# Kernel optimization log

Measured on AMD Instinct MI355X. Metric: run time of the kernel, lower is better.

Reference implementation:

```python
import jax, jax.numpy as jnp
import numpy as np

B, L = 8, 2048
AMP, ANG = 48, 16
H = 4
AQK, GQK = 12, 6   # amp/ang qk head dims
AV, GV = 12, 6     # amp/ang v head dims
LOOKBACK = 100


def setup_inputs() -> dict:
    key = jax.random.key(0)
    ks = jax.random.split(key, 16)
    def w(k, i, o):
        # kaiming-uniform-ish scale; stored [in, out] so forward is x @ W
        bound = 1.0 / np.sqrt(i)
        return jax.random.uniform(k, (i, o), jnp.float32, -bound, bound)
    return dict(
        x_ang=jax.random.normal(ks[0], (B, L, 2 * ANG), jnp.float32),
        x_amp=jax.random.normal(ks[1], (B, L, AMP), jnp.float32),
        Wq_amp=w(ks[2], AMP, H * AQK),
        Wk_amp=w(ks[3], AMP, H * AQK),
        Wv_amp=w(ks[4], AMP, H * AV),
        Wq_ang_r=w(ks[5], ANG, H * GQK),
        Wq_ang_i=w(ks[6], ANG, H * GQK),
        Wk_ang_r=w(ks[7], ANG, H * GQK),
        Wk_ang_i=w(ks[8], ANG, H * GQK),
        Wv_ang_r=w(ks[9], ANG, H * GV),
        Wv_ang_i=w(ks[10], ANG, H * GV),
        Wout_amp=w(ks[11], H * AV, AMP),
        bout_amp=jax.random.uniform(ks[12], (AMP,), jnp.float32, -0.1, 0.1),
        Wout_ang_r=w(ks[13], H * GV, ANG),
        Wout_ang_i=w(ks[14], H * GV, ANG),
    )


def _clin(xr, xi, Wr, Wi):
    # complex linear: (xr + i xi) @ (Wr + i Wi)
    return xr @ Wr - xi @ Wi, xr @ Wi + xi @ Wr


def reference(x_ang, x_amp, Wq_amp, Wk_amp, Wv_amp,
              Wq_ang_r, Wq_ang_i, Wk_ang_r, Wk_ang_i,
              Wv_ang_r, Wv_ang_i, Wout_amp, bout_amp,
              Wout_ang_r, Wout_ang_i):
    Bb, Ll, CA = x_ang.shape
    ang_r, ang_i = jnp.split(x_ang, 2, axis=-1)

    def heads(x, hd):  # [B,L,H*hd] -> [B,H,L,hd]
        return x.reshape(Bb, Ll, H, hd).transpose(0, 2, 1, 3)

    q_amp = heads(x_amp @ Wq_amp, AQK)
    k_amp = heads(x_amp @ Wk_amp, AQK)
    qar, qai = _clin(ang_r, ang_i, Wq_ang_r, Wq_ang_i)
    kar, kai = _clin(ang_r, ang_i, Wk_ang_r, Wk_ang_i)
    q = jnp.concatenate([heads(qar, GQK), heads(qai, GQK), q_amp], axis=-1)  # [B,H,L,24]
    k = jnp.concatenate([heads(kar, GQK), heads(kai, GQK), k_amp], axis=-1)

    v_amp = heads(x_amp @ Wv_amp, AV)
    var, vai = _clin(ang_r, ang_i, Wv_ang_r, Wv_ang_i)
    v = jnp.concatenate([heads(var, GV), heads(vai, GV), v_amp], axis=-1)  # [B,H,L,24]

    scale = 1.0 / jnp.sqrt(jnp.asarray(q.shape[-1], q.dtype))
    scores = jnp.einsum('bhqd,bhkd->bhqk', q, k) * scale
    idx = jnp.arange(Ll)
    valid = (idx[None, :] <= idx[:, None]) & (idx[None, :] >= idx[:, None] - (LOOKBACK - 1))
    mask = jnp.where(valid, jnp.asarray(0.0, scores.dtype), jnp.finfo(scores.dtype).min)
    attn = jax.nn.softmax(scores + mask, axis=-1)
    out = jnp.einsum('bhqk,bhkd->bhqd', attn, v)  # [B,H,L,24]

    o_ang_r, o_ang_i, o_amp = jnp.split(out, [GV, 2 * GV], axis=-1)

    def merge(x):  # [B,H,L,hd] -> [B,L,H*hd]
        return x.transpose(0, 2, 1, 3).reshape(Bb, Ll, -1)

    out_amp = merge(o_amp) @ Wout_amp + bout_amp
    out_ang_r, out_ang_i = _clin(merge(o_ang_r), merge(o_ang_i), Wout_ang_r, Wout_ang_i)
    return (out_ang_r, out_ang_i, out_amp)
```

## Files before the change

### kernel.cpp

```cpp
#include <hip/hip_runtime.h>
#include <hip/hip_bf16.h>

constexpr int B = 8;
constexpr int L = 2048;
constexpr int ANG = 16;
constexpr int AMP = 48;
constexpr int H = 4;
constexpr int AQK = 12, GQK = 6;
constexpr int AV = 12, GV = 6;
constexpr int HD = 2 * GQK + AQK;
constexpr int LOOKBACK = 100;
constexpr int NTOK = B * L;

constexpr int TQ     = 64;
constexpr int GROUPS = 4;
constexpr int CHUNK  = 25;
constexpr int MAXK   = TQ + LOOKBACK - 1;
constexpr int NT     = L / TQ;

struct StageT {
    float xam[MAXK][49];
    float xan[MAXK][33];
};
struct TileT {
    float4 Ks[MAXK][8];
    float4 Vs[MAXK][8];
    float4 Qs[TQ][7];
};
union SharedU { StageT stage; TileT t; };

__global__ __launch_bounds__(256, 3) void fused_qkv_attn3_kernel(
    const float* __restrict__ x_ang, const float* __restrict__ x_amp,
    const float* __restrict__ Wq_amp, const float* __restrict__ Wk_amp,
    const float* __restrict__ Wv_amp,
    const float* __restrict__ Wq_ang_r, const float* __restrict__ Wq_ang_i,
    const float* __restrict__ Wk_ang_r, const float* __restrict__ Wk_ang_i,
    const float* __restrict__ Wv_ang_r, const float* __restrict__ Wv_ang_i,
    float* __restrict__ att)
{
    __shared__ SharedU u;

    const int tid = threadIdx.x;
    const int bh  = blockIdx.x / NT;
    const int qt  = blockIdx.x % NT;
    const int b   = bh / H, h = bh % H;
    const int q0  = qt * TQ;
    int kmin = q0 - (LOOKBACK - 1); if (kmin < 0) kmin = 0;
    const int nrows = q0 + TQ - kmin;
    const int qoff  = q0 - kmin;

    {
        const float4* xm4 = (const float4*)(x_amp + ((size_t)b * L + kmin) * AMP);
        const float4* xg4 = (const float4*)(x_ang + ((size_t)b * L + kmin) * (2 * ANG));
        int namp = nrows * 12;
        int ntot = namp + nrows * 8;
        for (int c = tid; c < ntot; c += 256) {
            if (c < namp) {
                int r = c / 12, i = c % 12;
                float4 t = xm4[c];
                float* p = &u.stage.xam[r][4 * i];
                p[0] = t.x; p[1] = t.y; p[2] = t.z; p[3] = t.w;
            } else {
                int c2 = c - namp;
                int r = c2 / 8, i = c2 % 8;
                float4 t = xg4[c2];
                float* p = &u.stage.xan[r][4 * i];
                p[0] = t.x; p[1] = t.y; p[2] = t.z; p[3] = t.w;
            }
        }
    }
    __syncthreads();

    float4 kpack[6], vpack[6], qpack[6];
    const bool kvact = (tid < nrows);
    const bool qact  = (tid >= 192);
    const int  qrow  = tid - 192;

    #pragma unroll
    for (int s = 0; s < 6; ++s) {
        if (kvact) {
            int r = tid;
            if (s >= 3) {
                int col4 = h * AQK + (s - 3) * 4;
                const float* Wk = Wk_amp + col4;
                const float* Wv = Wv_amp + col4;
                float4 ka = {0,0,0,0}, va = {0,0,0,0};
                #pragma unroll
                for (int i = 0; i < AMP; ++i) {
                    float x = u.stage.xam[r][i];
                    float4 wk = *(const float4*)(Wk + i * 48);
                    float4 wv = *(const float4*)(Wv + i * 48);
                    ka.x += x * wk.x; ka.y += x * wk.y; ka.z += x * wk.z; ka.w += x * wk.w;
                    va.x += x * wv.x; va.y += x * wv.y; va.z += x * wv.z; va.w += x * wv.w;
                }
                kpack[s] = ka; vpack[s] = va;
            } else {
                float kk[4], vv[4];
                #pragma unroll
                for (int c = 0; c < 4; ++c) {
                    int d = 4 * s + c;
                    bool re = (d < GQK);
                    int dd = re ? d : d - GQK;
                    int col = h * GQK + dd;
                    const float* WkA = re ? Wk_ang_r : Wk_ang_i;
                    const float* WkB = re ? Wk_ang_i : Wk_ang_r;
                    const float* WvA = re ? Wv_ang_r : Wv_ang_i;
                    const float* WvB = re ? Wv_ang_i : Wv_ang_r;
                    float sgn = re ? -1.f : 1.f;
                    float ak = 0, bk = 0, aw = 0, bw = 0;
                    #pragma unroll
                    for (int i = 0; i < ANG; ++i) {
                        float xr = u.stage.xan[r][i];
                        float xi = u.stage.xan[r][16 + i];
                        ak += xr * WkA[i * 24 + col];  bk += xi * WkB[i * 24 + col];
                        aw += xr * WvA[i * 24 + col];  bw += xi * WvB[i * 24 + col];
                    }
                    kk[c] = ak + sgn * bk;  vv[c] = aw + sgn * bw;
                }
                kpack[s] = make_float4(kk[0], kk[1], kk[2], kk[3]);
                vpack[s] = make_float4(vv[0], vv[1], vv[2], vv[3]);
            }
        }
        if (qact) {
            int r = qoff + qrow;
            if (s >= 3) {
                int col4 = h * AQK + (s - 3) * 4;
                const float* Wq = Wq_amp + col4;
                float4 qa = {0,0,0,0};
                #pragma unroll
                for (int i = 0; i < AMP; ++i) {
                    float x = u.stage.xam[r][i];
                    float4 wq = *(const float4*)(Wq + i * 48);
                    qa.x += x * wq.x; qa.y += x * wq.y; qa.z += x * wq.z; qa.w += x * wq.w;
                }
                qpack[s] = qa;
            } else {
                float qq[4];
                #pragma unroll
                for (int c = 0; c < 4; ++c) {
                    int d = 4 * s + c;
                    bool re = (d < GQK);
                    int dd = re ? d : d - GQK;
                    int col = h * GQK + dd;
                    const float* WA = re ? Wq_ang_r : Wq_ang_i;
                    const float* WB = re ? Wq_ang_i : Wq_ang_r;
                    float sgn = re ? -1.f : 1.f;
                    float aa = 0, bb = 0;
                    #pragma unroll
                    for (int i = 0; i < ANG; ++i) {
                        float xr = u.stage.xan[r][i];
                        float xi = u.stage.xan[r][16 + i];
                        aa += xr * WA[i * 24 + col];  bb += xi * WB[i * 24 + col];
                    }
                    qq[c] = aa + sgn * bb;
                }
                qpack[s] = make_float4(qq[0], qq[1], qq[2], qq[3]);
            }
        }
    }
    __syncthreads();

    if (kvact) {
        int r = tid, rx = r & 7;
        #pragma unroll
        for (int s = 0; s < 6; ++s) {
            u.t.Ks[r][s ^ rx] = kpack[s];
            u.t.Vs[r][s ^ rx] = vpack[s];
        }
    } else if (tid < MAXK) {
        float4 z = make_float4(0.f,0.f,0.f,0.f);
        #pragma unroll
        for (int s = 0; s < 6; ++s) { u.t.Ks[tid][s] = z; u.t.Vs[tid][s] = z; }
    }
    if (qact) {
        #pragma unroll
        for (int s = 0; s < 6; ++s) u.t.Qs[qrow][s] = qpack[s];
    }
    __syncthreads();

    const int lane = tid & 63;
    const int w    = tid >> 6;
    const int q16  = lane & 15;
    const int g    = lane >> 4;
    const int ql   = w * 16 + q16;
    const int qi   = q0 + ql;

    float4 q4[6];
    #pragma unroll
    for (int s = 0; s < 6; ++s) q4[s] = u.t.Qs[ql][s];

    const float scale = 0.2041241452319315f;
    int j0 = qi - (LOOKBACK - 1); if (j0 < 0) j0 = 0;
    const int jstart = j0 + g;

    float sc[CHUNK];
    #pragma unroll
    for (int t = 0; t < CHUNK; ++t) {
        int j  = jstart + t * GROUPS;
        int r  = j - kmin;
        int rx = r & 7;
        float d = 0.f;
        #pragma unroll
        for (int s = 0; s < 6; ++s) {
            float4 kk = u.t.Ks[r][s ^ rx];
            d += q4[s].x*kk.x + q4[s].y*kk.y + q4[s].z*kk.z + q4[s].w*kk.w;
        }
        sc[t] = (j <= qi) ? d * scale : -3.0e38f;
    }
    float m = sc[0];
    #pragma unroll
    for (int t = 1; t < CHUNK; ++t) m = fmaxf(m, sc[t]);
    float ssum = 0.f;
    #pragma unroll
    for (int t = 0; t < CHUNK; ++t) {
        float p = __expf(sc[t] - m);
        p = (sc[t] > -1.0e37f) ? p : 0.f;
        sc[t] = p;
        ssum += p;
    }
    float4 o[6];
    #pragma unroll
    for (int s = 0; s < 6; ++s) o[s] = make_float4(0.f,0.f,0.f,0.f);
    #pragma unroll
    for (int t = 0; t < CHUNK; ++t) {
        float p  = sc[t];
        int j    = jstart + t * GROUPS;
        int r    = j - kmin;
        int rx   = r & 7;
        #pragma unroll
        for (int s = 0; s < 6; ++s) {
            float4 vv = u.t.Vs[r][s ^ rx];
            o[s].x += p * vv.x; o[s].y += p * vv.y;
            o[s].z += p * vv.z; o[s].w += p * vv.w;
        }
    }

    #pragma unroll
    for (int d = 16; d <= 32; d <<= 1) {
        float m2 = __shfl_xor(m, d);
        float s2 = __shfl_xor(ssum, d);
        float mm = fmaxf(m, m2);
        float c1 = __expf(m - mm);
        float c2 = __expf(m2 - mm);
        ssum = ssum * c1 + s2 * c2;
        #pragma unroll
        for (int s = 0; s < 6; ++s) {
            o[s].x = o[s].x * c1 + __shfl_xor(o[s].x, d) * c2;
            o[s].y = o[s].y * c1 + __shfl_xor(o[s].y, d) * c2;
            o[s].z = o[s].z * c1 + __shfl_xor(o[s].z, d) * c2;
            o[s].w = o[s].w * c1 + __shfl_xor(o[s].w, d) * c2;
        }
        m = mm;
    }
    float inv = 1.f / ssum;

    {
        float4* dst = (float4*)att + (size_t)(b * L + qi) * 24 + h * 6;
        if (g == 0) {
            dst[0] = make_float4(o[0].x*inv, o[0].y*inv, o[0].z*inv, o[0].w*inv);
            dst[4] = make_float4(o[4].x*inv, o[4].y*inv, o[4].z*inv, o[4].w*inv);
        } else if (g == 1) {
            dst[1] = make_float4(o[1].x*inv, o[1].y*inv, o[1].z*inv, o[1].w*inv);
            dst[5] = make_float4(o[5].x*inv, o[5].y*inv, o[5].z*inv, o[5].w*inv);
        } else if (g == 2) {
            dst[2] = make_float4(o[2].x*inv, o[2].y*inv, o[2].z*inv, o[2].w*inv);
        } else {
            dst[3] = make_float4(o[3].x*inv, o[3].y*inv, o[3].z*inv, o[3].w*inv);
        }
    }
}

constexpr int PJ_AMP_BLOCKS = (NTOK * 12) / 256;
constexpr int PJ_ANG_BLOCKS = (NTOK * 4) / 256;

__global__ __launch_bounds__(256) void proj4_kernel(
    const float* __restrict__ att,
    const float* __restrict__ Wout_amp, const float* __restrict__ bout_amp,
    const float* __restrict__ Wout_ang_r, const float* __restrict__ Wout_ang_i,
    float* __restrict__ out)
{
    constexpr size_t ANG_OUT = (size_t)NTOK * ANG;
    int bid = blockIdx.x;

    if (bid < PJ_AMP_BLOCKS) {
        int gidx = bid * 256 + threadIdx.x;
        int c4   = (gidx % 12) * 4;
        int tok  = gidx / 12;
        const float4* at4 = (const float4*)att + (size_t)tok * 24;

        float a[48];
        #pragma unroll
        for (int h = 0; h < H; ++h) {
            #pragma unroll
            for (int i = 0; i < 3; ++i) {
                float4 t = at4[h * 6 + 3 + i];
                a[h*12 + 4*i+0]=t.x; a[h*12 + 4*i+1]=t.y;
                a[h*12 + 4*i+2]=t.z; a[h*12 + 4*i+3]=t.w;
            }
        }
        float4 acc = *(const float4*)(bout_amp + c4);
        #pragma unroll
        for (int i = 0; i < 48; ++i) {
            float4 w = *(const float4*)(Wout_amp + i * 48 + c4);
            acc.x += a[i]*w.x; acc.y += a[i]*w.y; acc.z += a[i]*w.z; acc.w += a[i]*w.w;
        }
        *(float4*)(out + 2*ANG_OUT + (size_t)tok * 48 + c4) = acc;
    } else {
        int gidx = (bid - PJ_AMP_BLOCKS) * 256 + threadIdx.x;
        int c4   = (gidx % 4) * 4;
        int tok  = gidx / 4;
        const float4* at4 = (const float4*)att + (size_t)tok * 24;

        float ar[24], ai[24];
        #pragma unroll
        for (int h = 0; h < H; ++h) {
            float4 t0 = at4[h*6+0], t1 = at4[h*6+1], t2 = at4[h*6+2];
            ar[h*6+0]=t0.x; ar[h*6+1]=t0.y; ar[h*6+2]=t0.z; ar[h*6+3]=t0.w;
            ar[h*6+4]=t1.x; ar[h*6+5]=t1.y;
            ai[h*6+0]=t1.z; ai[h*6+1]=t1.w;
            ai[h*6+2]=t2.x; ai[h*6+3]=t2.y; ai[h*6+4]=t2.z; ai[h*6+5]=t2.w;
        }
        float4 accr = make_float4(0.f,0.f,0.f,0.f);
        float4 acci = make_float4(0.f,0.f,0.f,0.f);
        #pragma unroll
        for (int i = 0; i < 24; ++i) {
            float4 wr = *(const float4*)(Wout_ang_r + i * 16 + c4);
            float4 wi = *(const float4*)(Wout_ang_i + i * 16 + c4);
            float r = ar[i], im = ai[i];
            accr.x += r*wr.x - im*wi.x;  accr.y += r*wr.y - im*wi.y;
            accr.z += r*wr.z - im*wi.z;  accr.w += r*wr.w - im*wi.w;
            acci.x += r*wi.x + im*wr.x;  acci.y += r*wi.y + im*wr.y;
            acci.z += r*wi.z + im*wr.z;  acci.w += r*wi.w + im*wr.w;
        }
        *(float4*)(out + (size_t)tok * 16 + c4)           = accr;
        *(float4*)(out + ANG_OUT + (size_t)tok * 16 + c4) = acci;
    }
}

extern "C" void kernel_launch(void* const* d_in, const int* in_sizes, int n_in,
                              void* d_out, int out_size, void* d_ws, size_t ws_size,
                              hipStream_t stream)
{
    const float* x_ang      = (const float*)d_in[0];
    const float* x_amp      = (const float*)d_in[1];
    const float* Wq_amp     = (const float*)d_in[2];
    const float* Wk_amp     = (const float*)d_in[3];
    const float* Wv_amp     = (const float*)d_in[4];
    const float* Wq_ang_r   = (const float*)d_in[5];
    const float* Wq_ang_i   = (const float*)d_in[6];
    const float* Wk_ang_r   = (const float*)d_in[7];
    const float* Wk_ang_i   = (const float*)d_in[8];
    const float* Wv_ang_r   = (const float*)d_in[9];
    const float* Wv_ang_i   = (const float*)d_in[10];
    const float* Wout_amp   = (const float*)d_in[11];
    const float* bout_amp   = (const float*)d_in[12];
    const float* Wout_ang_r = (const float*)d_in[13];
    const float* Wout_ang_i = (const float*)d_in[14];

    float* out = (float*)d_out;
    float* att = (float*)d_ws;

    fused_qkv_attn3_kernel<<<B * H * NT, 256, 0, stream>>>(
        x_ang, x_amp, Wq_amp, Wk_amp, Wv_amp,
        Wq_ang_r, Wq_ang_i, Wk_ang_r, Wk_ang_i, Wv_ang_r, Wv_ang_i,
        att);

    proj4_kernel<<<PJ_AMP_BLOCKS + PJ_ANG_BLOCKS, 256, 0, stream>>>(
        att, Wout_amp, bout_amp, Wout_ang_r, Wout_ang_i, out);
}
```

Baseline: 149.5 us.

## Store staged inputs and K/V tiles in fp16 to shrink LDS footprint

Inputs staged in LDS are converted to packed fp16 (round-toward-zero), and K/V tiles are stored as packed fp16 in 3 float4 slots per row instead of 6 fp32 slots with XOR swizzle. Projections are rewritten into a shared per-row helper, and the launch bound is raised to 4 blocks per SM. The aim is to cut LDS usage and traffic so more blocks fit, and to halve K/V shared reads. The cost is reduced precision from fp16 truncation of inputs and K/V, plus extra conversion instructions and possible register pressure under the tighter launch bound.

```diff
diff --git a/kernel.cpp b/kernel.cpp
--- a/kernel.cpp
+++ b/kernel.cpp
@@ -1,5 +1,6 @@
 #include <hip/hip_runtime.h>
 #include <hip/hip_bf16.h>
+#include <hip/hip_fp16.h>
 
 constexpr int B = 8;
 constexpr int L = 2048;
@@ -12,24 +13,71 @@
 constexpr int LOOKBACK = 100;
 constexpr int NTOK = B * L;
 
+typedef __fp16 f16x2 __attribute__((ext_vector_type(2)));
+
+__device__ inline f16x2 pkrtz(float a, float b) {
+    return __builtin_amdgcn_cvt_pkrtz(a, b);
+}
+__device__ inline float2 up2(f16x2 v) { return make_float2((float)v[0], (float)v[1]); }
+
+union F4H { float4 v; f16x2 h[4]; };
+
 constexpr int TQ     = 64;
 constexpr int GROUPS = 4;
 constexpr int CHUNK  = 25;
 constexpr int MAXK   = TQ + LOOKBACK - 1;
 constexpr int NT     = L / TQ;
 
-struct StageT {
-    float xam[MAXK][49];
-    float xan[MAXK][33];
-};
-struct TileT {
-    float4 Ks[MAXK][8];
-    float4 Vs[MAXK][8];
+struct StageT { f16x2 xall[MAXK][41]; };
+struct TileT  {
+    float4 Ks[MAXK][3];
+    float4 Vs[MAXK][3];
     float4 Qs[TQ][7];
 };
-union SharedU { StageT stage; TileT t; };
-
-__global__ __launch_bounds__(256, 3) void fused_qkv_attn3_kernel(
+union SharedU { StageT s; TileT t; };
+
+__device__ inline void proj_row(const f16x2* __restrict__ xrow, int h,
+                                const float* __restrict__ Wamp,
+                                const float* __restrict__ Wang_r,
+                                const float* __restrict__ Wang_i,
+                                float out[24])
+{
+    float a[12];
+    #pragma unroll
+    for (int c = 0; c < 12; ++c) a[c] = 0.f;
+    #pragma unroll
+    for (int i2 = 0; i2 < 24; ++i2) {
+        float2 x2 = up2(xrow[i2]);
+        const float* w0 = Wamp + (2 * i2) * 48 + h * AQK;
+        const float* w1 = Wamp + (2 * i2 + 1) * 48 + h * AQK;
+        #pragma unroll
+        for (int c = 0; c < 12; ++c)
+            a[c] += x2.x * w0[c] + x2.y * w1[c];
+    }
+    float rr[6], im[6];
+    #pragma unroll
+    for (int c = 0; c < 6; ++c) { rr[c] = 0.f; im[c] = 0.f; }
+    #pragma unroll
+    for (int i2 = 0; i2 < 8; ++i2) {
+        float2 xr2 = up2(xrow[24 + i2]);
+        float2 xi2 = up2(xrow[32 + i2]);
+        const float* wr0 = Wang_r + (2 * i2) * 24 + h * GQK;
+        const float* wi0 = Wang_i + (2 * i2) * 24 + h * GQK;
+        const float* wr1 = Wang_r + (2 * i2 + 1) * 24 + h * GQK;
+        const float* wi1 = Wang_i + (2 * i2 + 1) * 24 + h * GQK;
+        #pragma unroll
+        for (int c = 0; c < 6; ++c) {
+            rr[c] += xr2.x * wr0[c] - xi2.x * wi0[c] + xr2.y * wr1[c] - xi2.y * wi1[c];
+            im[c] += xr2.x * wi0[c] + xi2.x * wr0[c] + xr2.y * wi1[c] + xi2.y * wr1[c];
+        }
+    }
+    #pragma unroll
+    for (int c = 0; c < 6; ++c) { out[c] = rr[c]; out[6 + c] = im[c]; }
+    #pragma unroll
+    for (int c = 0; c < 12; ++c) out[12 + c] = a[c];
+}
+
+__global__ __launch_bounds__(256, 4) void fused_qkv_attn4_kernel(
     const float* __restrict__ x_ang, const float* __restrict__ x_amp,
     const float* __restrict__ Wq_amp, const float* __restrict__ Wk_amp,
     const float* __restrict__ Wv_amp,
@@ -57,124 +105,58 @@
         for (int c = tid; c < ntot; c += 256) {
             if (c < namp) {
                 int r = c / 12, i = c % 12;
-                float4 t = xm4[c];
-                float* p = &u.stage.xam[r][4 * i];
-                p[0] = t.x; p[1] = t.y; p[2] = t.z; p[3] = t.w;
+                float4 t4 = xm4[c];
+                u.s.xall[r][2 * i]     = pkrtz(t4.x, t4.y);
+                u.s.xall[r][2 * i + 1] = pkrtz(t4.z, t4.w);
             } else {
                 int c2 = c - namp;
                 int r = c2 / 8, i = c2 % 8;
-                float4 t = xg4[c2];
-                float* p = &u.stage.xan[r][4 * i];
-                p[0] = t.x; p[1] = t.y; p[2] = t.z; p[3] = t.w;
+                float4 t4 = xg4[c2];
+                u.s.xall[r][24 + 2 * i]     = pkrtz(t4.x, t4.y);
+                u.s.xall[r][24 + 2 * i + 1] = pkrtz(t4.z, t4.w);
             }
         }
     }
     __syncthreads();
 
-    float4 kpack[6], vpack[6], qpack[6];
     const bool kvact = (tid < nrows);
     const bool qact  = (tid >= 192);
     const int  qrow  = tid - 192;
 
-    #pragma unroll
-    for (int s = 0; s < 6; ++s) {
-        if (kvact) {
-            int r = tid;
-            if (s >= 3) {
-                int col4 = h * AQK + (s - 3) * 4;
-                const float* Wk = Wk_amp + col4;
-                const float* Wv = Wv_amp + col4;
-                float4 ka = {0,0,0,0}, va = {0,0,0,0};
-                #pragma unroll
-                for (int i = 0; i < AMP; ++i) {
-                    float x = u.stage.xam[r][i];
-                    float4 wk = *(const float4*)(Wk + i * 48);
-                    float4 wv = *(const float4*)(Wv + i * 48);
-                    ka.x += x * wk.x; ka.y += x * wk.y; ka.z += x * wk.z; ka.w += x * wk.w;
-                    va.x += x * wv.x; va.y += x * wv.y; va.z += x * wv.z; va.w += x * wv.w;
-                }
-                kpack[s] = ka; vpack[s] = va;
-            } else {
-                float kk[4], vv[4];
-                #pragma unroll
-                for (int c = 0; c < 4; ++c) {
-                    int d = 4 * s + c;
-                    bool re = (d < GQK);
-                    int dd = re ? d : d - GQK;
-                    int col = h * GQK + dd;
-                    const float* WkA = re ? Wk_ang_r : Wk_ang_i;
-                    const float* WkB = re ? Wk_ang_i : Wk_ang_r;
-                    const float* WvA = re ? Wv_ang_r : Wv_ang_i;
-                    const float* WvB = re ? Wv_ang_i : Wv_ang_r;
-                    float sgn = re ? -1.f : 1.f;
-                    float ak = 0, bk = 0, aw = 0, bw = 0;
-                    #pragma unroll
-                    for (int i = 0; i < ANG; ++i) {
-                        float xr = u.stage.xan[r][i];
-                        float xi = u.stage.xan[r][16 + i];
-                        ak += xr * WkA[i * 24 + col];  bk += xi * WkB[i * 24 + col];
-                        aw += xr * WvA[i * 24 + col];  bw += xi * WvB[i * 24 + col];
-                    }
-                    kk[c] = ak + sgn * bk;  vv[c] = aw + sgn * bw;
-                }
-                kpack[s] = make_float4(kk[0], kk[1], kk[2], kk[3]);
-                vpack[s] = make_float4(vv[0], vv[1], vv[2], vv[3]);
+    float kd[24], vd[24], qd[24];
+    if (kvact) {
+        const f16x2* xrow = u.s.xall[tid];
+        proj_row(xrow, h, Wk_amp, Wk_ang_r, Wk_ang_i, kd);
+        proj_row(xrow, h, Wv_amp, Wv_ang_r, Wv_ang_i, vd);
+    }
+    if (qact) {
+        const f16x2* xrow = u.s.xall[qoff + qrow];
+        proj_row(xrow, h, Wq_amp, Wq_ang_r, Wq_ang_i, qd);
+    }
+    __syncthreads();
+
+    if (kvact) {
+        int r = tid;
+        #pragma unroll
+        for (int sl = 0; sl < 3; ++sl) {
+            F4H pk_, pv_;
+            #pragma unroll
+            for (int j = 0; j < 4; ++j) {
+                pk_.h[j] = pkrtz(kd[8 * sl + 2 * j], kd[8 * sl + 2 * j + 1]);
+                pv_.h[j] = pkrtz(vd[8 * sl + 2 * j], vd[8 * sl + 2 * j + 1]);
             }
-        }
-        if (qact) {
-            int r = qoff + qrow;
-            if (s >= 3) {
-                int col4 = h * AQK + (s - 3) * 4;
-                const float* Wq = Wq_amp + col4;
-                float4 qa = {0,0,0,0};
-                #pragma unroll
-                for (int i = 0; i < AMP; ++i) {
-                    float x = u.stage.xam[r][i];
-                    float4 wq = *(const float4*)(Wq + i * 48);
-                    qa.x += x * wq.x; qa.y += x * wq.y; qa.z += x * wq.z; qa.w += x * wq.w;
-                }
-                qpack[s] = qa;
-            } else {
-                float qq[4];
-                #pragma unroll
-                for (int c = 0; c < 4; ++c) {
-                    int d = 4 * s + c;
-                    bool re = (d < GQK);
-                    int dd = re ? d : d - GQK;
-                    int col = h * GQK + dd;
-                    const float* WA = re ? Wq_ang_r : Wq_ang_i;
-                    const float* WB = re ? Wq_ang_i : Wq_ang_r;
-                    float sgn = re ? -1.f : 1.f;
-                    float aa = 0, bb = 0;
-                    #pragma unroll
-                    for (int i = 0; i < ANG; ++i) {
-                        float xr = u.stage.xan[r][i];
-                        float xi = u.stage.xan[r][16 + i];
-                        aa += xr * WA[i * 24 + col];  bb += xi * WB[i * 24 + col];
-                    }
-                    qq[c] = aa + sgn * bb;
-                }
-                qpack[s] = make_float4(qq[0], qq[1], qq[2], qq[3]);
-            }
-        }
-    }
-    __syncthreads();
-
-    if (kvact) {
-        int r = tid, rx = r & 7;
-        #pragma unroll
-        for (int s = 0; s < 6; ++s) {
-            u.t.Ks[r][s ^ rx] = kpack[s];
-            u.t.Vs[r][s ^ rx] = vpack[s];
+            u.t.Ks[r][sl] = pk_.v;
+            u.t.Vs[r][sl] = pv_.v;
         }
     } else if (tid < MAXK) {
-        float4 z = make_float4(0.f,0.f,0.f,0.f);
-        #pragma unroll
-        for (int s = 0; s < 6; ++s) { u.t.Ks[tid][s] = z; u.t.Vs[tid][s] = z; }
+        float4 z = make_float4(0.f, 0.f, 0.f, 0.f);
+        #pragma unroll
+        for (int sl = 0; sl < 3; ++sl) { u.t.Ks[tid][sl] = z; u.t.Vs[tid][sl] = z; }
     }
     if (qact) {
         #pragma unroll
-        for (int s = 0; s < 6; ++s) u.t.Qs[qrow][s] = qpack[s];
+        for (int s = 0; s < 6; ++s)
+            u.t.Qs[qrow][s] = make_float4(qd[4*s], qd[4*s+1], qd[4*s+2], qd[4*s+3]);
     }
     __syncthreads();
 
@@ -185,9 +167,12 @@
     const int ql   = w * 16 + q16;
     const int qi   = q0 + ql;
 
-    float4 q4[6];
-    #pragma unroll
-    for (int s = 0; s < 6; ++s) q4[s] = u.t.Qs[ql][s];
+    float qf[24];
+    #pragma unroll
+    for (int s = 0; s < 6; ++s) {
+        float4 t4 = u.t.Qs[ql][s];
+        qf[4*s] = t4.x; qf[4*s+1] = t4.y; qf[4*s+2] = t4.z; qf[4*s+3] = t4.w;
+    }
 
     const float scale = 0.2041241452319315f;
     int j0 = qi - (LOOKBACK - 1); if (j0 < 0) j0 = 0;
@@ -196,14 +181,16 @@
     float sc[CHUNK];
     #pragma unroll
     for (int t = 0; t < CHUNK; ++t) {
-        int j  = jstart + t * GROUPS;
-        int r  = j - kmin;
-        int rx = r & 7;
+        int j = jstart + t * GROUPS;
+        int r = j - kmin;
+        F4H k0, k1, k2;
+        k0.v = u.t.Ks[r][0]; k1.v = u.t.Ks[r][1]; k2.v = u.t.Ks[r][2];
         float d = 0.f;
         #pragma unroll
-        for (int s = 0; s < 6; ++s) {
-            float4 kk = u.t.Ks[r][s ^ rx];
-            d += q4[s].x*kk.x + q4[s].y*kk.y + q4[s].z*kk.z + q4[s].w*kk.w;
+        for (int jj = 0; jj < 4; ++jj) {
+            float2 a0 = up2(k0.h[jj]); d += a0.x * qf[2*jj]      + a0.y * qf[2*jj+1];
+            float2 a1 = up2(k1.h[jj]); d += a1.x * qf[8 + 2*jj]  + a1.y * qf[8 + 2*jj+1];
+            float2 a2 = up2(k2.h[jj]); d += a2.x * qf[16 + 2*jj] + a2.y * qf[16 + 2*jj+1];
         }
         sc[t] = (j <= qi) ? d * scale : -3.0e38f;
     }
@@ -218,20 +205,21 @@
         sc[t] = p;
         ssum += p;
     }
-    float4 o[6];
-    #pragma unroll
-    for (int s = 0; s < 6; ++s) o[s] = make_float4(0.f,0.f,0.f,0.f);
+    float o[24];
+    #pragma unroll
+    for (int e = 0; e < 24; ++e) o[e] = 0.f;
     #pragma unroll
     for (int t = 0; t < CHUNK; ++t) {
-        float p  = sc[t];
-        int j    = jstart + t * GROUPS;
-        int r    = j - kmin;
-        int rx   = r & 7;
-        #pragma unroll
-        for (int s = 0; s < 6; ++s) {
-            float4 vv = u.t.Vs[r][s ^ rx];
-            o[s].x += p * vv.x; o[s].y += p * vv.y;
-            o[s].z += p * vv.z; o[s].w += p * vv.w;
+        float p = sc[t];
+        int j = jstart + t * GROUPS;
+        int r = j - kmin;
+        F4H v0, v1, v2;
+        v0.v = u.t.Vs[r][0]; v1.v = u.t.Vs[r][1]; v2.v = u.t.Vs[r][2];
+        #pragma unroll
+        for (int jj = 0; jj < 4; ++jj) {
+            float2 a0 = up2(v0.h[jj]); o[2*jj]      += p * a0.x; o[2*jj+1]      += p * a0.y;
+            float2 a1 = up2(v1.h[jj]); o[8 + 2*jj]  += p * a1.x; o[8 + 2*jj+1]  += p * a1.y;
+            float2 a2 = up2(v2.h[jj]); o[16 + 2*jj] += p * a2.x; o[16 + 2*jj+1] += p * a2.y;
         }
     }
 
@@ -244,12 +232,8 @@
         float c2 = __expf(m2 - mm);
         ssum = ssum * c1 + s2 * c2;
         #pragma unroll
-        for (int s = 0; s < 6; ++s) {
-            o[s].x = o[s].x * c1 + __shfl_xor(o[s].x, d) * c2;
-            o[s].y = o[s].y * c1 + __shfl_xor(o[s].y, d) * c2;
-            o[s].z = o[s].z * c1 + __shfl_xor(o[s].z, d) * c2;
-            o[s].w = o[s].w * c1 + __shfl_xor(o[s].w, d) * c2;
-        }
+        for (int e = 0; e < 24; ++e)
+            o[e] = o[e] * c1 + __shfl_xor(o[e], d) * c2;
         m = mm;
     }
     float inv = 1.f / ssum;
@@ -257,15 +241,15 @@
     {
         float4* dst = (float4*)att + (size_t)(b * L + qi) * 24 + h * 6;
         if (g == 0) {
-            dst[0] = make_float4(o[0].x*inv, o[0].y*inv, o[0].z*inv, o[0].w*inv);
-            dst[4] = make_float4(o[4].x*inv, o[4].y*inv, o[4].z*inv, o[4].w*inv);
+            dst[0] = make_float4(o[0]*inv,  o[1]*inv,  o[2]*inv,  o[3]*inv);
+            dst[4] = make_float4(o[16]*inv, o[17]*inv, o[18]*inv, o[19]*inv);
         } else if (g == 1) {
-            dst[1] = make_float4(o[1].x*inv, o[1].y*inv, o[1].z*inv, o[1].w*inv);
-            dst[5] = make_float4(o[5].x*inv, o[5].y*inv, o[5].z*inv, o[5].w*inv);
+            dst[1] = make_float4(o[4]*inv,  o[5]*inv,  o[6]*inv,  o[7]*inv);
+            dst[5] = make_float4(o[20]*inv, o[21]*inv, o[22]*inv, o[23]*inv);
         } else if (g == 2) {
-            dst[2] = make_float4(o[2].x*inv, o[2].y*inv, o[2].z*inv, o[2].w*inv);
+            dst[2] = make_float4(o[8]*inv,  o[9]*inv,  o[10]*inv, o[11]*inv);
         } else {
-            dst[3] = make_float4(o[3].x*inv, o[3].y*inv, o[3].z*inv, o[3].w*inv);
+            dst[3] = make_float4(o[12]*inv, o[13]*inv, o[14]*inv, o[15]*inv);
         }
     }
 }
@@ -360,7 +344,7 @@
     float* out = (float*)d_out;
     float* att = (float*)d_ws;
 
-    fused_qkv_attn3_kernel<<<B * H * NT, 256, 0, stream>>>(
+    fused_qkv_attn4_kernel<<<B * H * NT, 256, 0, stream>>>(
         x_ang, x_amp, Wq_amp, Wk_amp, Wv_amp,
         Wq_ang_r, Wq_ang_i, Wk_ang_r, Wk_ang_i, Wv_ang_r, Wv_ang_i,
         att);
```

Measured after the change: 297.8 us. +99.2%, slower.
